# Optimization experiments

Measured on AMD Instinct MI355X. Metric: run time of the kernel, lower is better.

The kernel has to match this reference:

```python
import jax, jax.numpy as jnp
import numpy as np
from jax import lax

L = 2048        # leaves per tree
VOCAB = 50000
IN_DIM = 300
MEM = 150
HID = 50
NCLS = 5


def _balanced_tree(n_leaf):
    # children-before-parent topological order; node ids: [0, n_leaf) leaves,
    # [n_leaf, 2*n_leaf-1) internal, last id is the root's single child (ROOT is passthrough).
    level = list(range(n_leaf)); nid = n_leaf; lefts = []; rights = []
    while len(level) > 1:
        nxt = []
        for j in range(0, len(level) - 1, 2):
            lefts.append(level[j]); rights.append(level[j + 1]); nxt.append(nid); nid += 1
        if len(level) % 2:
            nxt.append(level[-1])
        level = nxt
    return np.asarray(lefts, np.int32), np.asarray(rights, np.int32)


def setup_inputs() -> dict:
    key = jax.random.key(0)
    ks = jax.random.split(key, 12)
    left, right = _balanced_tree(L)
    s = 0.05
    return {
        "l_tokens": jax.random.randint(ks[0], (L,), 0, VOCAB, dtype=jnp.int32),
        "r_tokens": jax.random.randint(ks[1], (L,), 0, VOCAB, dtype=jnp.int32),
        "left_idx": jnp.asarray(left),
        "right_idx": jnp.asarray(right),
        "emb": jax.random.normal(ks[2], (VOCAB, IN_DIM), jnp.float32) * s,
        "W_ioux": jax.random.normal(ks[3], (IN_DIM, 3 * MEM), jnp.float32) * s,
        "b_ioux": jnp.zeros((3 * MEM,), jnp.float32),
        "W_iouh": jax.random.normal(ks[4], (MEM, 3 * MEM), jnp.float32) * s,
        "b_iouh": jnp.zeros((3 * MEM,), jnp.float32),
        "W_fx": jax.random.normal(ks[5], (IN_DIM, MEM), jnp.float32) * s,
        "b_fx": jnp.zeros((MEM,), jnp.float32),
        "W_fh": jax.random.normal(ks[6], (MEM, MEM), jnp.float32) * s,
        "b_fh": jnp.zeros((MEM,), jnp.float32),
        "W_attn": jax.random.normal(ks[7], (2 * MEM, MEM), jnp.float32) * s,
        "b_attn": jnp.zeros((MEM,), jnp.float32),
        "W_wh": jax.random.normal(ks[8], (2 * MEM, HID), jnp.float32) * s,
        "b_wh": jnp.zeros((HID,), jnp.float32),
        "W_wp": jax.random.normal(ks[9], (HID, NCLS), jnp.float32) * s,
        "b_wp": jnp.zeros((NCLS,), jnp.float32),
    }


def _gates(iou):
    i, o, u = jnp.split(iou, 3, axis=-1)
    return jax.nn.sigmoid(i), jax.nn.sigmoid(o), jnp.tanh(u)


def _tree_lstm(tokens, left, right, emb, W_ioux, b_ioux, W_iouh, b_iouh, W_fh, b_fh):
    # Leaves (child_c = child_h = 0): iou = ioux(x) + iouh(0); fc term vanishes.
    x = emb[tokens]                                   # [L, in_dim]
    i, o, u = _gates(x @ W_ioux + b_ioux + b_iouh)
    c_leaf = i * u
    h_leaf = o * jnp.tanh(c_leaf)
    n_leaf = tokens.shape[0]
    N = 2 * n_leaf - 1
    C = jnp.zeros((N, MEM), x.dtype).at[:n_leaf].set(c_leaf)
    H = jnp.zeros((N, MEM), x.dtype).at[:n_leaf].set(h_leaf)

    # Internal nodes (inputs=None branch): iou = iouh(sum h_child); f_k = sigmoid(fh(h_k)).
    def step(carry, inp):
        C, H = carry
        k, li, ri = inp
        hl, hr = H[li], H[ri]
        i, o, u = _gates((hl + hr) @ W_iouh + b_iouh)
        fl = jax.nn.sigmoid(hl @ W_fh + b_fh)
        fr = jax.nn.sigmoid(hr @ W_fh + b_fh)
        c = i * u + fl * C[li] + fr * C[ri]
        h = o * jnp.tanh(c)
        return (C.at[k].set(c), H.at[k].set(h)), None

    ids = jnp.arange(n_leaf, N, dtype=jnp.int32)
    (C, H), _ = lax.scan(step, (C, H), (ids, left, right))
    return H  # [N, MEM]; H[-1] is the root hidden state (ROOT is passthrough)


def reference(l_tokens, r_tokens, left_idx, right_idx, emb, W_ioux, b_ioux, W_iouh, b_iouh, W_fx, b_fx, W_fh, b_fh, W_attn, b_attn, W_wh, b_wh, W_wp, b_wp):
    Hl = _tree_lstm(l_tokens, left_idx, right_idx, emb, W_ioux, b_ioux, W_iouh, b_iouh, W_fh, b_fh)
    Hr = _tree_lstm(r_tokens, left_idx, right_idx, emb, W_ioux, b_ioux, W_iouh, b_iouh, W_fh, b_fh)
    # Soft cross-attention over all node hidden states (torch code builds [Nr,Nl,m] beta;
    # here expressed as matmuls -- identical math).
    scores = Hl @ Hr.T                               # [Nl, Nr]
    beta_sum = jax.nn.softmax(scores, axis=1) @ Hr    # [Nl, MEM]
    alpha_sum = jax.nn.softmax(scores.T, axis=1) @ Hl  # [Nr, MEM]
    v_l = jnp.concatenate([Hl, beta_sum], axis=1) @ W_attn + b_attn
    v_r = jnp.concatenate([Hr, alpha_sum], axis=1) @ W_attn + b_attn
    lh = v_l[-1:]  # root hidden (root_idx is the root's matched row)
    rh = v_r[-1:]
    feats = jnp.concatenate([lh * rh, jnp.abs(lh - rh)], axis=1)
    hid = jax.nn.sigmoid(feats @ W_wh + b_wh)
    return jax.nn.log_softmax(hid @ W_wp + b_wp, axis=-1)  # [1, NCLS]
```

## Files before the change

kernel.cpp:

```cpp
#include <hip/hip_runtime.h>
#include <math.h>

#define LEAVES 2048
#define NN     4095
#define MEMD   150
#define IOUD   450
#define IND    300
#define STR    152
#define CT     4096


__device__ __forceinline__ float sigf(float x) { return 1.f / (1.f + expf(-x)); }

__global__ __launch_bounds__(320) void k_leaf(
    const int* __restrict__ ltok, const int* __restrict__ rtok,
    const float* __restrict__ emb, const float* __restrict__ Wx,
    const float* __restrict__ bx, const float* __restrict__ bh,
    float* __restrict__ C, float* __restrict__ H)
{
    __shared__ float xs[IND][8];
    __shared__ int   tok[8];
    const int tree = blockIdx.y, t = threadIdx.x;
    const int leaf0 = blockIdx.x << 3;
    const int* toks = tree ? rtok : ltok;

    if (t < 8) tok[t] = toks[leaf0 + t];
    __syncthreads();
    for (int idx = t; idx < 600; idx += 320) {
        int q = idx >> 3, m = idx & 7;
        float4 v = *(const float4*)(emb + (size_t)tok[m] * IND + 4 * q);
        xs[4*q+0][m] = v.x; xs[4*q+1][m] = v.y;
        xs[4*q+2][m] = v.z; xs[4*q+3][m] = v.w;
    }
    __syncthreads();

    if (t >= 300) return;
    const int hf = (t >= 150) ? 1 : 0;
    const int d  = t - 150 * hf;
    const int m0 = hf * 4;

    const float bi = bx[d]       + bh[d];
    const float bo = bx[d + 150] + bh[d + 150];
    const float bu = bx[d + 300] + bh[d + 300];
    float ai[4] = {bi,bi,bi,bi}, ao[4] = {bo,bo,bo,bo}, au[4] = {bu,bu,bu,bu};

    const float* wp = Wx + d;
    #pragma unroll 4
    for (int k = 0; k < IND; ++k) {
        float wi = wp[k * IOUD];
        float wo = wp[k * IOUD + 150];
        float wu = wp[k * IOUD + 300];
        float4 x4 = *(const float4*)(&xs[k][m0]);
        float xv[4] = {x4.x, x4.y, x4.z, x4.w};
        #pragma unroll
        for (int m = 0; m < 4; ++m) {
            ai[m] = fmaf(xv[m], wi, ai[m]);
            ao[m] = fmaf(xv[m], wo, ao[m]);
            au[m] = fmaf(xv[m], wu, au[m]);
        }
    }

    float* Ct = C + ((size_t)tree * CT + leaf0 + m0) * STR;
    float* Ht = H + ((size_t)tree * CT + leaf0 + m0) * STR;
    #pragma unroll
    for (int m = 0; m < 4; ++m) {
        float c = sigf(ai[m]) * tanhf(au[m]);
        float h = sigf(ao[m]) * tanhf(c);
        Ct[(size_t)m * STR + d] = c;
        Ht[(size_t)m * STR + d] = h;
    }
}

template<int M>
__global__ __launch_bounds__(320) void k_lvl(
    const float* __restrict__ Wh, const float* __restrict__ bh,
    const float* __restrict__ Wf, const float* __restrict__ bf,
    float* __restrict__ C, float* __restrict__ H, int PB, int CB)
{
    __shared__ float buf[MEMD][4 * M];
    const int tree = blockIdx.y, t = threadIdx.x;
    const int p0 = blockIdx.x * 2 * M;
    float* Ct = C + (size_t)tree * CT * STR;
    float* Ht = H + (size_t)tree * CT * STR;

    for (int idx = t; idx < 2 * M * MEMD; idx += 320) {
        int m = idx / MEMD, d2 = idx - m * MEMD;
        int cc = CB + 2 * (p0 + m);
        float a = Ht[(size_t)cc * STR + d2];
        float b = Ht[(size_t)(cc + 1) * STR + d2];
        buf[d2][2*m + 0] = a + b;
        buf[d2][2*m + 1] = a;
    }
    __syncthreads();

    if (t >= 300) return;
    const int hf = (t >= 150) ? 1 : 0;
    const int d  = t - 150 * hf;
    const int m0 = hf * M;

    const float bi = bh[d], bo = bh[d + 150], bu = bh[d + 300], bfv = bf[d];
    float ai[M], ao[M], au[M], afs[M], afl[M];
    #pragma unroll
    for (int m = 0; m < M; ++m) {
        ai[m] = bi; ao[m] = bo; au[m] = bu; afs[m] = 2.f * bfv; afl[m] = bfv;
    }

    const float* whp = Wh + d;
    const float* wfp = Wf + d;
    #pragma unroll 4
    for (int k = 0; k < MEMD; ++k) {
        float wi = whp[k * IOUD];
        float wo = whp[k * IOUD + 150];
        float wu = whp[k * IOUD + 300];
        float wf = wfp[k * MEMD];
        float pair[2 * M];
        if (M == 2) {
            float4 p4 = *(const float4*)(&buf[k][2 * m0]);
            pair[0] = p4.x; pair[1] = p4.y; pair[2] = p4.z; pair[3] = p4.w;
        } else {
            float2 p2 = *(const float2*)(&buf[k][2 * m0]);
            pair[0] = p2.x; pair[1] = p2.y;
        }
        #pragma unroll
        for (int m = 0; m < M; ++m) {
            float hs = pair[2*m], hl = pair[2*m + 1];
            ai[m]  = fmaf(hs, wi, ai[m]);
            ao[m]  = fmaf(hs, wo, ao[m]);
            au[m]  = fmaf(hs, wu, au[m]);
            afs[m] = fmaf(hs, wf, afs[m]);
            afl[m] = fmaf(hl, wf, afl[m]);
        }
    }

    #pragma unroll
    for (int m = 0; m < M; ++m) {
        int p = p0 + m0 + m;
        int cc = CB + 2 * p;
        float cl = Ct[(size_t)cc * STR + d];
        float cr = Ct[(size_t)(cc + 1) * STR + d];
        float frv = afs[m] - afl[m];
        float c = sigf(ai[m]) * tanhf(au[m]) + sigf(afl[m]) * cl + sigf(frv) * cr;
        float h = sigf(ao[m]) * tanhf(c);
        size_t rw = (size_t)(PB + p) * STR + d;
        Ct[rw] = c;
        Ht[rw] = h;
    }
}

__global__ __launch_bounds__(640) void k_node(
    const float* __restrict__ Wh, const float* __restrict__ bh,
    const float* __restrict__ Wf, const float* __restrict__ bf,
    float* __restrict__ C, float* __restrict__ H, int PB, int CB)
{
    __shared__ float hsv[MEMD], hlv[MEMD];
    __shared__ float part[4][5][152];
    const int tree = blockIdx.y, node = blockIdx.x, t = threadIdx.x;
    float* Ct = C + (size_t)tree * CT * STR;
    float* Ht = H + (size_t)tree * CT * STR;
    const int c0 = CB + 2 * node;

    if (t < MEMD) {
        float a = Ht[(size_t)c0 * STR + t];
        float b = Ht[(size_t)(c0 + 1) * STR + t];
        hsv[t] = a + b;
        hlv[t] = a;
    }
    __syncthreads();

    const int grp = t / 160, d = t - grp * 160;
    if (d < MEMD) {
        const int k0 = (grp * MEMD) >> 2;
        const int k1 = ((grp + 1) * MEMD) >> 2;
        float ai = 0.f, ao = 0.f, au = 0.f, afs = 0.f, afl = 0.f;
        const float* whp = Wh + d;
        const float* wfp = Wf + d;
        #pragma unroll 4
        for (int k = k0; k < k1; ++k) {
            float wi = whp[k * IOUD];
            float wo = whp[k * IOUD + 150];
            float wu = whp[k * IOUD + 300];
            float wf = wfp[k * MEMD];
            float hs = hsv[k], hl = hlv[k];
            ai  = fmaf(hs, wi, ai);
            ao  = fmaf(hs, wo, ao);
            au  = fmaf(hs, wu, au);
            afs = fmaf(hs, wf, afs);
            afl = fmaf(hl, wf, afl);
        }
        part[grp][0][d] = ai;  part[grp][1][d] = ao;  part[grp][2][d] = au;
        part[grp][3][d] = afs; part[grp][4][d] = afl;
    }
    __syncthreads();

    if (t < MEMD) {
        const int d2 = t;
        float ai = bh[d2], ao = bh[d2 + 150], au = bh[d2 + 300];
        float bfv = bf[d2];
        float afs = 2.f * bfv, afl = bfv;
        #pragma unroll
        for (int g = 0; g < 4; ++g) {
            ai  += part[g][0][d2]; ao  += part[g][1][d2]; au += part[g][2][d2];
            afs += part[g][3][d2]; afl += part[g][4][d2];
        }
        float cl = Ct[(size_t)c0 * STR + d2];
        float cr = Ct[(size_t)(c0 + 1) * STR + d2];
        float frv = afs - afl;
        float c = sigf(ai) * tanhf(au) + sigf(afl) * cl + sigf(frv) * cr;
        float h = sigf(ao) * tanhf(c);
        size_t rw = (size_t)(PB + node) * STR + d2;
        Ct[rw] = c;
        Ht[rw] = h;
    }
}

__global__ __launch_bounds__(256) void k_attn(
    const float* __restrict__ H, float* __restrict__ cstat, float* __restrict__ part)
{
    __shared__ float lv[MEMD];
    __shared__ float sc[64];
    __shared__ float pv[64];
    const int bid = blockIdx.x, t = threadIdx.x;
    const int side = bid >> 6, chunk = bid & 63;
    const int j0 = chunk << 6;
    const int jn = min(64, NN - j0);
    const float* lastrow = H + ((size_t)side * CT + (NN - 1)) * STR;
    if (t < MEMD) lv[t] = lastrow[t];
    __syncthreads();

    const float* src = H + (size_t)(side ^ 1) * CT * STR + (size_t)j0 * STR;
    const int wave = t >> 6, lane = t & 63;
    for (int r = wave; r < jn; r += 4) {
        const float* row = src + (size_t)r * STR;
        float a = lv[lane] * row[lane] + lv[lane + 64] * row[lane + 64];
        if (lane < 22) a += lv[lane + 128] * row[lane + 128];
        #pragma unroll
        for (int off = 32; off; off >>= 1) a += __shfl_xor(a, off);
        if (lane == 0) sc[r] = a;
    }
    __syncthreads();
    if (wave == 0) {
        float v = (lane < jn) ? sc[lane] : -3.4e38f;
        float m = v;
        #pragma unroll
        for (int off = 32; off; off >>= 1) m = fmaxf(m, __shfl_xor(m, off));
        float e = (lane < jn) ? expf(v - m) : 0.f;
        pv[lane] = e;
        float s = e;
        #pragma unroll
        for (int off = 32; off; off >>= 1) s += __shfl_xor(s, off);
        if (lane == 0) {
            cstat[(side * 64 + chunk) * 2 + 0] = m;
            cstat[(side * 64 + chunk) * 2 + 1] = s;
        }
    }
    __syncthreads();
    if (t < MEMD) {
        float a = 0.f;
        for (int j = 0; j < jn; ++j) a += pv[j] * src[(size_t)j * STR + t];
        part[(size_t)(side * 64 + chunk) * STR + t] = a;
    }
}

__global__ __launch_bounds__(512) void k_final(
    const float* __restrict__ H, const float* __restrict__ cstat,
    const float* __restrict__ part,
    const float* __restrict__ Wattn, const float* __restrict__ battn,
    const float* __restrict__ Wwh, const float* __restrict__ bwh,
    const float* __restrict__ Wwp, const float* __restrict__ bwp,
    float* __restrict__ outp)
{
    __shared__ float scl[2][64];
    __shared__ float gseS[2];
    __shared__ float ba[300], catl[300], catr[300], vl[150], vr[150];
    __shared__ float feats[300], hid[50], logits[5];
    const int t = threadIdx.x, wave = t >> 6, lane = t & 63;

    if (wave < 2) {
        float lm = cstat[(wave * 64 + lane) * 2 + 0];
        float ls = cstat[(wave * 64 + lane) * 2 + 1];
        float m = lm;
        #pragma unroll
        for (int off = 32; off; off >>= 1) m = fmaxf(m, __shfl_xor(m, off));
        float s = expf(lm - m);
        scl[wave][lane] = s;
        float se = ls * s;
        #pragma unroll
        for (int off = 32; off; off >>= 1) se += __shfl_xor(se, off);
        if (lane == 0) gseS[wave] = se;
    }
    __syncthreads();
    if (t < 300) {
        int side = t / MEMD, d = t - side * MEMD;
        float a = 0.f;
        for (int c = 0; c < 64; ++c)
            a += part[(size_t)(side * 64 + c) * STR + d] * scl[side][c];
        ba[t] = a / gseS[side];
    }
    __syncthreads();
    const float* Hl_last = H + (size_t)(0 * CT + NN - 1) * STR;
    const float* Hr_last = H + (size_t)(1 * CT + NN - 1) * STR;
    if (t < MEMD) {
        catl[t] = Hl_last[t]; catl[150 + t] = ba[t];
        catr[t] = Hr_last[t]; catr[150 + t] = ba[150 + t];
    }
    __syncthreads();
    if (t < 300) {
        int d = (t < 150) ? t : t - 150;
        const float* cat = (t < 150) ? catl : catr;
        float a = battn[d];
        for (int k = 0; k < 300; ++k) a = fmaf(cat[k], Wattn[k * 150 + d], a);
        if (t < 150) vl[d] = a; else vr[d] = a;
    }
    __syncthreads();
    if (t < MEMD) {
        feats[t] = vl[t] * vr[t];
        feats[150 + t] = fabsf(vl[t] - vr[t]);
    }
    __syncthreads();
    if (t < 50) {
        float a = bwh[t];
        for (int k = 0; k < 300; ++k) a = fmaf(feats[k], Wwh[k * 50 + t], a);
        hid[t] = sigf(a);
    }
    __syncthreads();
    if (t < 5) {
        float a = bwp[t];
        for (int g = 0; g < 50; ++g) a = fmaf(hid[g], Wwp[g * 5 + t], a);
        logits[t] = a;
    }
    __syncthreads();
    if (t == 0) {
        float m = logits[0];
        for (int c = 1; c < 5; ++c) m = fmaxf(m, logits[c]);
        float s = 0.f;
        for (int c = 0; c < 5; ++c) s += expf(logits[c] - m);
        float lse = m + logf(s);
        for (int c = 0; c < 5; ++c) outp[c] = logits[c] - lse;
    }
}

extern "C" void kernel_launch(void* const* d_in, const int* in_sizes, int n_in,
                              void* d_out, int out_size, void* d_ws, size_t ws_size,
                              hipStream_t stream)
{
    const int*   ltok  = (const int*)d_in[0];
    const int*   rtok  = (const int*)d_in[1];
    const float* emb   = (const float*)d_in[4];
    const float* Wx    = (const float*)d_in[5];
    const float* bx    = (const float*)d_in[6];
    const float* Wh    = (const float*)d_in[7];
    const float* bh    = (const float*)d_in[8];
    const float* Wf    = (const float*)d_in[11];
    const float* bf    = (const float*)d_in[12];
    const float* Wattn = (const float*)d_in[13];
    const float* battn = (const float*)d_in[14];
    const float* Wwh   = (const float*)d_in[15];
    const float* bwh   = (const float*)d_in[16];
    const float* Wwp   = (const float*)d_in[17];
    const float* bwp   = (const float*)d_in[18];
    float* out = (float*)d_out;

    float* ws   = (float*)d_ws;
    float* C    = ws;
    float* H    = C + (size_t)2 * CT * STR;
    float* cs   = H + (size_t)2 * CT * STR;
    float* part = cs + 256;

    k_leaf<<<dim3(256, 2), dim3(320), 0, stream>>>(ltok, rtok, emb, Wx, bx, bh, C, H);

    k_lvl<2><<<dim3(256, 2), dim3(320), 0, stream>>>(Wh, bh, Wf, bf, C, H, 2048, 0);
    k_lvl<1><<<dim3(256, 2), dim3(320), 0, stream>>>(Wh, bh, Wf, bf, C, H, 3072, 2048);
    k_lvl<1><<<dim3(128, 2), dim3(320), 0, stream>>>(Wh, bh, Wf, bf, C, H, 3584, 3072);

    k_node<<<dim3(128, 2), dim3(640), 0, stream>>>(Wh, bh, Wf, bf, C, H, 3840, 3584);
    k_node<<<dim3(64,  2), dim3(640), 0, stream>>>(Wh, bh, Wf, bf, C, H, 3968, 3840);
    k_node<<<dim3(32,  2), dim3(640), 0, stream>>>(Wh, bh, Wf, bf, C, H, 4032, 3968);
    k_node<<<dim3(16,  2), dim3(640), 0, stream>>>(Wh, bh, Wf, bf, C, H, 4064, 4032);
    k_node<<<dim3(8,   2), dim3(640), 0, stream>>>(Wh, bh, Wf, bf, C, H, 4080, 4064);
    k_node<<<dim3(4,   2), dim3(640), 0, stream>>>(Wh, bh, Wf, bf, C, H, 4088, 4080);
    k_node<<<dim3(2,   2), dim3(640), 0, stream>>>(Wh, bh, Wf, bf, C, H, 4092, 4088);
    k_node<<<dim3(1,   2), dim3(640), 0, stream>>>(Wh, bh, Wf, bf, C, H, 4094, 4092);

    k_attn<<<dim3(128), dim3(256), 0, stream>>>(H, cs, part);
    k_final<<<dim3(1), dim3(512), 0, stream>>>(H, cs, part, Wattn, battn,
                                               Wwh, bwh, Wwp, bwp, out);
}
```

Before: 159.2 us.

## Split K-reduction across two thread halves in leaf and level kernels

The leaf and lower-level tree-LSTM kernels now run 640 threads per block, splitting the reduction dimension in half between two thread groups and combining the partial sums through shared memory before the gate nonlinearities. k_lvl drops its template, always handling 2 parents per half-block, so the 2nd and 3rd level launches use half as many blocks. The goal is a shorter serial dependency chain per thread and more wavefronts to hide weight-load latency. The cost is an extra shared-memory partial buffer, a block sync, and fewer blocks on the later levels.

```diff
diff --git a/kernel.cpp b/kernel.cpp
--- a/kernel.cpp
+++ b/kernel.cpp
@@ -12,7 +12,7 @@
 
 __device__ __forceinline__ float sigf(float x) { return 1.f / (1.f + expf(-x)); }
 
-__global__ __launch_bounds__(320) void k_leaf(
+__global__ __launch_bounds__(640) void k_leaf(
     const int* __restrict__ ltok, const int* __restrict__ rtok,
     const float* __restrict__ emb, const float* __restrict__ Wx,
     const float* __restrict__ bx, const float* __restrict__ bh,
@@ -20,71 +20,97 @@
 {
     __shared__ float xs[IND][8];
     __shared__ int   tok[8];
+    __shared__ float pb[300][13];
     const int tree = blockIdx.y, t = threadIdx.x;
     const int leaf0 = blockIdx.x << 3;
     const int* toks = tree ? rtok : ltok;
 
     if (t < 8) tok[t] = toks[leaf0 + t];
     __syncthreads();
-    for (int idx = t; idx < 600; idx += 320) {
-        int q = idx >> 3, m = idx & 7;
+    if (t < 600) {
+        int q = t >> 3, m = t & 7;
         float4 v = *(const float4*)(emb + (size_t)tok[m] * IND + 4 * q);
         xs[4*q+0][m] = v.x; xs[4*q+1][m] = v.y;
         xs[4*q+2][m] = v.z; xs[4*q+3][m] = v.w;
     }
     __syncthreads();
 
-    if (t >= 300) return;
-    const int hf = (t >= 150) ? 1 : 0;
-    const int d  = t - 150 * hf;
+    const int kh = (t >= 320) ? 1 : 0;
+    const int tt = t - 320 * kh;
+    const bool act = (tt < 300);
+    const int hf = (tt >= 150) ? 1 : 0;
+    const int d  = tt - 150 * hf;
     const int m0 = hf * 4;
 
-    const float bi = bx[d]       + bh[d];
-    const float bo = bx[d + 150] + bh[d + 150];
-    const float bu = bx[d + 300] + bh[d + 300];
-    float ai[4] = {bi,bi,bi,bi}, ao[4] = {bo,bo,bo,bo}, au[4] = {bu,bu,bu,bu};
-
-    const float* wp = Wx + d;
-    #pragma unroll 4
-    for (int k = 0; k < IND; ++k) {
-        float wi = wp[k * IOUD];
-        float wo = wp[k * IOUD + 150];
-        float wu = wp[k * IOUD + 300];
-        float4 x4 = *(const float4*)(&xs[k][m0]);
-        float xv[4] = {x4.x, x4.y, x4.z, x4.w};
+    float ai[4], ao[4], au[4];
+    if (act) {
+        if (kh == 0) {
+            const float bi = bx[d]       + bh[d];
+            const float bo = bx[d + 150] + bh[d + 150];
+            const float bu = bx[d + 300] + bh[d + 300];
+            #pragma unroll
+            for (int m = 0; m < 4; ++m) { ai[m] = bi; ao[m] = bo; au[m] = bu; }
+        } else {
+            #pragma unroll
+            for (int m = 0; m < 4; ++m) { ai[m] = 0.f; ao[m] = 0.f; au[m] = 0.f; }
+        }
+        const float* wp = Wx + d;
+        const int kb = kh * 150;
+        #pragma unroll 5
+        for (int kk = 0; kk < 150; ++kk) {
+            const int k = kb + kk;
+            float wi = wp[k * IOUD];
+            float wo = wp[k * IOUD + 150];
+            float wu = wp[k * IOUD + 300];
+            float4 x4 = *(const float4*)(&xs[k][m0]);
+            float xv[4] = {x4.x, x4.y, x4.z, x4.w};
+            #pragma unroll
+            for (int m = 0; m < 4; ++m) {
+                ai[m] = fmaf(xv[m], wi, ai[m]);
+                ao[m] = fmaf(xv[m], wo, ao[m]);
+                au[m] = fmaf(xv[m], wu, au[m]);
+            }
+        }
+    }
+    if (kh == 1 && act) {
         #pragma unroll
         for (int m = 0; m < 4; ++m) {
-            ai[m] = fmaf(xv[m], wi, ai[m]);
-            ao[m] = fmaf(xv[m], wo, ao[m]);
-            au[m] = fmaf(xv[m], wu, au[m]);
-        }
-    }
-
-    float* Ct = C + ((size_t)tree * CT + leaf0 + m0) * STR;
-    float* Ht = H + ((size_t)tree * CT + leaf0 + m0) * STR;
-    #pragma unroll
-    for (int m = 0; m < 4; ++m) {
-        float c = sigf(ai[m]) * tanhf(au[m]);
-        float h = sigf(ao[m]) * tanhf(c);
-        Ct[(size_t)m * STR + d] = c;
-        Ht[(size_t)m * STR + d] = h;
-    }
-}
-
-template<int M>
-__global__ __launch_bounds__(320) void k_lvl(
+            pb[tt][3*m + 0] = ai[m];
+            pb[tt][3*m + 1] = ao[m];
+            pb[tt][3*m + 2] = au[m];
+        }
+    }
+    __syncthreads();
+    if (kh == 0 && act) {
+        float* Ct = C + ((size_t)tree * CT + leaf0 + m0) * STR;
+        float* Ht = H + ((size_t)tree * CT + leaf0 + m0) * STR;
+        #pragma unroll
+        for (int m = 0; m < 4; ++m) {
+            float aiv = ai[m] + pb[tt][3*m + 0];
+            float aov = ao[m] + pb[tt][3*m + 1];
+            float auv = au[m] + pb[tt][3*m + 2];
+            float c = sigf(aiv) * tanhf(auv);
+            float h = sigf(aov) * tanhf(c);
+            Ct[(size_t)m * STR + d] = c;
+            Ht[(size_t)m * STR + d] = h;
+        }
+    }
+}
+
+__global__ __launch_bounds__(640) void k_lvl(
     const float* __restrict__ Wh, const float* __restrict__ bh,
     const float* __restrict__ Wf, const float* __restrict__ bf,
     float* __restrict__ C, float* __restrict__ H, int PB, int CB)
 {
-    __shared__ float buf[MEMD][4 * M];
+    __shared__ float buf[MEMD][8];
+    __shared__ float pb[300][11];
     const int tree = blockIdx.y, t = threadIdx.x;
-    const int p0 = blockIdx.x * 2 * M;
+    const int p0 = blockIdx.x * 4;
     float* Ct = C + (size_t)tree * CT * STR;
     float* Ht = H + (size_t)tree * CT * STR;
 
-    for (int idx = t; idx < 2 * M * MEMD; idx += 320) {
-        int m = idx / MEMD, d2 = idx - m * MEMD;
+    if (t < 600) {
+        int m = t / 150, d2 = t - m * 150;
         int cc = CB + 2 * (p0 + m);
         float a = Ht[(size_t)cc * STR + d2];
         float b = Ht[(size_t)(cc + 1) * STR + d2];
@@ -93,57 +119,76 @@
     }
     __syncthreads();
 
-    if (t >= 300) return;
-    const int hf = (t >= 150) ? 1 : 0;
-    const int d  = t - 150 * hf;
-    const int m0 = hf * M;
-
-    const float bi = bh[d], bo = bh[d + 150], bu = bh[d + 300], bfv = bf[d];
-    float ai[M], ao[M], au[M], afs[M], afl[M];
-    #pragma unroll
-    for (int m = 0; m < M; ++m) {
-        ai[m] = bi; ao[m] = bo; au[m] = bu; afs[m] = 2.f * bfv; afl[m] = bfv;
-    }
-
-    const float* whp = Wh + d;
-    const float* wfp = Wf + d;
-    #pragma unroll 4
-    for (int k = 0; k < MEMD; ++k) {
-        float wi = whp[k * IOUD];
-        float wo = whp[k * IOUD + 150];
-        float wu = whp[k * IOUD + 300];
-        float wf = wfp[k * MEMD];
-        float pair[2 * M];
-        if (M == 2) {
+    const int kh = (t >= 320) ? 1 : 0;
+    const int tt = t - 320 * kh;
+    const bool act = (tt < 300);
+    const int hf = (tt >= 150) ? 1 : 0;
+    const int d  = tt - 150 * hf;
+    const int m0 = hf * 2;
+
+    float ai[2], ao[2], au[2], afs[2], afl[2], cl[2], cr[2];
+    if (act) {
+        if (kh == 0) {
+            const float bi = bh[d], bo = bh[d + 150], bu = bh[d + 300], bfv = bf[d];
+            #pragma unroll
+            for (int m = 0; m < 2; ++m) {
+                ai[m] = bi; ao[m] = bo; au[m] = bu;
+                afs[m] = 2.f * bfv; afl[m] = bfv;
+                int cc = CB + 2 * (p0 + m0 + m);
+                cl[m] = Ct[(size_t)cc * STR + d];
+                cr[m] = Ct[(size_t)(cc + 1) * STR + d];
+            }
+        } else {
+            #pragma unroll
+            for (int m = 0; m < 2; ++m) {
+                ai[m] = 0.f; ao[m] = 0.f; au[m] = 0.f; afs[m] = 0.f; afl[m] = 0.f;
+            }
+        }
+        const float* whp = Wh + d;
+        const float* wfp = Wf + d;
+        const int kb = kh * 75;
+        #pragma unroll 5
+        for (int kk = 0; kk < 75; ++kk) {
+            const int k = kb + kk;
+            float wi = whp[k * IOUD];
+            float wo = whp[k * IOUD + 150];
+            float wu = whp[k * IOUD + 300];
+            float wf = wfp[k * MEMD];
             float4 p4 = *(const float4*)(&buf[k][2 * m0]);
-            pair[0] = p4.x; pair[1] = p4.y; pair[2] = p4.z; pair[3] = p4.w;
-        } else {
-            float2 p2 = *(const float2*)(&buf[k][2 * m0]);
-            pair[0] = p2.x; pair[1] = p2.y;
-        }
-        #pragma unroll
-        for (int m = 0; m < M; ++m) {
-            float hs = pair[2*m], hl = pair[2*m + 1];
-            ai[m]  = fmaf(hs, wi, ai[m]);
-            ao[m]  = fmaf(hs, wo, ao[m]);
-            au[m]  = fmaf(hs, wu, au[m]);
-            afs[m] = fmaf(hs, wf, afs[m]);
-            afl[m] = fmaf(hl, wf, afl[m]);
-        }
-    }
-
-    #pragma unroll
-    for (int m = 0; m < M; ++m) {
-        int p = p0 + m0 + m;
-        int cc = CB + 2 * p;
-        float cl = Ct[(size_t)cc * STR + d];
-        float cr = Ct[(size_t)(cc + 1) * STR + d];
-        float frv = afs[m] - afl[m];
-        float c = sigf(ai[m]) * tanhf(au[m]) + sigf(afl[m]) * cl + sigf(frv) * cr;
-        float h = sigf(ao[m]) * tanhf(c);
-        size_t rw = (size_t)(PB + p) * STR + d;
-        Ct[rw] = c;
-        Ht[rw] = h;
+            float hs0 = p4.x, hl0 = p4.y, hs1 = p4.z, hl1 = p4.w;
+            ai[0]  = fmaf(hs0, wi, ai[0]);   ai[1]  = fmaf(hs1, wi, ai[1]);
+            ao[0]  = fmaf(hs0, wo, ao[0]);   ao[1]  = fmaf(hs1, wo, ao[1]);
+            au[0]  = fmaf(hs0, wu, au[0]);   au[1]  = fmaf(hs1, wu, au[1]);
+            afs[0] = fmaf(hs0, wf, afs[0]);  afs[1] = fmaf(hs1, wf, afs[1]);
+            afl[0] = fmaf(hl0, wf, afl[0]);  afl[1] = fmaf(hl1, wf, afl[1]);
+        }
+    }
+    if (kh == 1 && act) {
+        #pragma unroll
+        for (int m = 0; m < 2; ++m) {
+            pb[tt][5*m + 0] = ai[m];
+            pb[tt][5*m + 1] = ao[m];
+            pb[tt][5*m + 2] = au[m];
+            pb[tt][5*m + 3] = afs[m];
+            pb[tt][5*m + 4] = afl[m];
+        }
+    }
+    __syncthreads();
+    if (kh == 0 && act) {
+        #pragma unroll
+        for (int m = 0; m < 2; ++m) {
+            float aiv  = ai[m]  + pb[tt][5*m + 0];
+            float aov  = ao[m]  + pb[tt][5*m + 1];
+            float auv  = au[m]  + pb[tt][5*m + 2];
+            float afsv = afs[m] + pb[tt][5*m + 3];
+            float aflv = afl[m] + pb[tt][5*m + 4];
+            float frv = afsv - aflv;
+            float c = sigf(aiv) * tanhf(auv) + sigf(aflv) * cl[m] + sigf(frv) * cr[m];
+            float h = sigf(aov) * tanhf(c);
+            size_t rw = (size_t)(PB + p0 + m0 + m) * STR + d;
+            Ct[rw] = c;
+            Ht[rw] = h;
+        }
     }
 }
 
@@ -366,11 +411,11 @@
     float* cs   = H + (size_t)2 * CT * STR;
     float* part = cs + 256;
 
-    k_leaf<<<dim3(256, 2), dim3(320), 0, stream>>>(ltok, rtok, emb, Wx, bx, bh, C, H);
-
-    k_lvl<2><<<dim3(256, 2), dim3(320), 0, stream>>>(Wh, bh, Wf, bf, C, H, 2048, 0);
-    k_lvl<1><<<dim3(256, 2), dim3(320), 0, stream>>>(Wh, bh, Wf, bf, C, H, 3072, 2048);
-    k_lvl<1><<<dim3(128, 2), dim3(320), 0, stream>>>(Wh, bh, Wf, bf, C, H, 3584, 3072);
+    k_leaf<<<dim3(256, 2), dim3(640), 0, stream>>>(ltok, rtok, emb, Wx, bx, bh, C, H);
+
+    k_lvl<<<dim3(256, 2), dim3(640), 0, stream>>>(Wh, bh, Wf, bf, C, H, 2048, 0);
+    k_lvl<<<dim3(128, 2), dim3(640), 0, stream>>>(Wh, bh, Wf, bf, C, H, 3072, 2048);
+    k_lvl<<<dim3(64,  2), dim3(640), 0, stream>>>(Wh, bh, Wf, bf, C, H, 3584, 3072);
 
     k_node<<<dim3(128, 2), dim3(640), 0, stream>>>(Wh, bh, Wf, bf, C, H, 3840, 3584);
     k_node<<<dim3(64,  2), dim3(640), 0, stream>>>(Wh, bh, Wf, bf, C, H, 3968, 3840);
```

Measured after the change: 150.9 us. 1.06x faster.
